# Kernel optimization log

Measured on AMD Instinct MI355X. Metric: run time of the kernel, lower is better.

## Reference

```python
import jax, jax.numpy as jnp
import numpy as np
import math

H = 16          # head_count
D = 1024        # model_dim
DT = 100        # topic_dim
DH = D // H     # dim_per_head


def _lin(x, W, b):
    return x @ W.T + b


def _shape(x, B):
    # [B, L, D] -> [B, H, L, DH]
    return x.reshape(B, -1, H, DH).transpose(0, 2, 1, 3)


def setup_inputs() -> dict:
    key = jax.random.key(0)
    ks = jax.random.split(key, 20)
    B, L = 4, 1024
    s = 0.02
    inp = {
        'key': jax.random.normal(ks[0], (B, L, D), jnp.float32),
        'value': jax.random.normal(ks[1], (B, L, D), jnp.float32),
        'query': jax.random.normal(ks[2], (B, L, D), jnp.float32),
        'mask': jax.random.randint(ks[3], (B, L, L), 0, 2).astype(bool),
        'topic_vec': jax.random.normal(ks[4], (B, L, DT), jnp.float32),
        'Wq': jax.random.normal(ks[5], (D, D), jnp.float32) * s,
        'bq': jnp.zeros((D,), jnp.float32),
        'Wk': jax.random.normal(ks[6], (D, D), jnp.float32) * s,
        'bk': jnp.zeros((D,), jnp.float32),
        'Wv': jax.random.normal(ks[7], (D, D), jnp.float32) * s,
        'bv': jnp.zeros((D,), jnp.float32),
        'Wtk': jax.random.normal(ks[8], (D, D), jnp.float32) * s,
        'btk': jnp.zeros((D,), jnp.float32),
        'Wtv': jax.random.normal(ks[9], (D, DT), jnp.float32) * s,
        'btv': jnp.zeros((D,), jnp.float32),
        'Wtw': jax.random.normal(ks[10], (H, 3 * D), jnp.float32) * s,
        'btw': jnp.zeros((H,), jnp.float32),
        'Wo': jax.random.normal(ks[11], (D, D), jnp.float32) * s,
        'bo': jnp.zeros((D,), jnp.float32),
    }
    return inp


def reference(key, value, query, mask, topic_vec,
              Wq, bq, Wk, bk, Wv, bv, Wtk, btk, Wtv, btv, Wtw, btw, Wo, bo):
    B = key.shape[0]
    # content and topic projections
    q_lin = _lin(query, Wq, bq)          # [B, L, D]
    k_lin = _lin(key, Wk, bk)
    v_lin = _lin(value, Wv, bv)
    tk_lin = _lin(key, Wtk, btk)         # topic keys from key states
    tv_lin = _lin(topic_vec, Wtv, btv)   # topic queries from topic distribution

    q = _shape(q_lin, B) / math.sqrt(DH)   # [B, H, Lq, DH]
    k = _shape(k_lin, B)
    v = _shape(v_lin, B)
    tk = _shape(tk_lin, B)
    tq = _shape(tv_lin, B) / math.sqrt(DH)

    scores = jnp.einsum('bhqd,bhkd->bhqk', q, k)          # content scores
    topic_scores = jnp.einsum('bhqd,bhkd->bhqk', tq, tk)  # topic scores

    # per-query, per-head mixing gate from concatenated projections (3*D -> H)
    gate = jax.nn.sigmoid(_lin(jnp.concatenate([q_lin, tk_lin, tv_lin], axis=-1), Wtw, btw))  # [B, L, H]
    p = gate.transpose(0, 2, 1)[..., None]                # [B, H, Lq, 1]
    scores = (1.0 - p) * scores + p * topic_scores

    # masked_fill(mask, -1e18), mask broadcast over heads
    scores = jnp.where(mask[:, None, :, :], -1e18, scores)
    attn = jax.nn.softmax(scores, axis=-1)
    # dropout is identity at eval time
    ctx = jnp.einsum('bhqk,bhkd->bhqd', attn, v)
    ctx = ctx.transpose(0, 2, 1, 3).reshape(B, -1, D)     # unshape
    return ctx @ Wo.T + bo
```

## Files before the change

### kernel.cpp

```cpp
#include <hip/hip_runtime.h>
#include <hip/hip_bf16.h>

#define BB 4
#define LL 1024
#define DD 1024
#define HH 16
#define DHH 64
#define DTT 100
#define ML (BB*LL)
#define LOG2E 1.4426950408889634f

typedef float f32x4 __attribute__((ext_vector_type(4)));
typedef short s16x8 __attribute__((ext_vector_type(8)));

__device__ __forceinline__ unsigned short f2bf(float x) {
    unsigned u = __builtin_bit_cast(unsigned, x);
    return (unsigned short)((u + 0x7FFFu + ((u >> 16) & 1u)) >> 16);
}
__device__ __forceinline__ unsigned short f2bf_fast(float x) {
    return (unsigned short)((__builtin_bit_cast(unsigned, x) + 0x8000u) >> 16);
}
__device__ __forceinline__ unsigned cvt_pk_bf16(float lo, float hi) {
    unsigned r;
    asm("v_cvt_pk_bf16_f32 %0, %1, %2" : "=v"(r) : "v"(lo), "v"(hi));
    return r;
}
__device__ __forceinline__ float bflo(unsigned u) { return __builtin_bit_cast(float, u << 16); }
__device__ __forceinline__ float bfhi(unsigned u) { return __builtin_bit_cast(float, u & 0xFFFF0000u); }
__device__ __forceinline__ int4 pack_bf16x8(float4 x0, float4 x1) {
    int4 o;
    o.x = cvt_pk_bf16(x0.x, x0.y); o.y = cvt_pk_bf16(x0.z, x0.w);
    o.z = cvt_pk_bf16(x1.x, x1.y); o.w = cvt_pk_bf16(x1.z, x1.w);
    return o;
}
__device__ __forceinline__ void gl_lds16(const unsigned short* g, char* l) {
    __builtin_amdgcn_global_load_lds(
        (const __attribute__((address_space(1))) unsigned*)g,
        (__attribute__((address_space(3))) unsigned*)l, 16, 0, 0);
}

__global__ __launch_bounds__(256)
void conv_fused(const float* __restrict__ qf, const float* __restrict__ kf,
                const float* __restrict__ vf,
                unsigned short* __restrict__ qb, unsigned short* __restrict__ kb,
                unsigned short* __restrict__ vb,
                const float* __restrict__ w0, const float* __restrict__ w1,
                const float* __restrict__ w2, const float* __restrict__ w3,
                const float* __restrict__ w4, unsigned short* __restrict__ wd,
                const float* __restrict__ wtw, unsigned short* __restrict__ wtwd,
                const float* __restrict__ wtv, unsigned short* __restrict__ wtvd,
                const float* __restrict__ topic, unsigned short* __restrict__ topicd,
                const int* __restrict__ mask, unsigned long long* __restrict__ MB) {
    const int bx0 = blockIdx.x, tid = threadIdx.x;
    if (bx0 < 6144) {
        const int which = bx0 >> 11;
        const float* src = which == 0 ? qf : (which == 1 ? kf : vf);
        unsigned short* dst = which == 0 ? qb : (which == 1 ? kb : vb);
        const int idx = (bx0 & 2047) * 256 + tid;
        float4 f0 = *(const float4*)(src + (size_t)idx * 8);
        float4 f1 = *(const float4*)(src + (size_t)idx * 8 + 4);
        *(int4*)(dst + (size_t)idx * 8) = pack_bf16x8(f0, f1);
        return;
    }
    const int bx = bx0 - 6144;
    if (bx < 2560) {
        const int which = bx >> 9;
        const float* src;
        switch (which) {
            case 0:  src = w0; break;
            case 1:  src = w1; break;
            case 2:  src = w2; break;
            case 3:  src = w3; break;
            default: src = w4; break;
        }
        unsigned short* dst = wd + (size_t)which * DD * DD;
        const int idx = (bx & 511) * 256 + tid;
        float4 f0 = *(const float4*)(src + (size_t)idx * 8);
        float4 f1 = *(const float4*)(src + (size_t)idx * 8 + 4);
        *(int4*)(dst + (size_t)idx * 8) = pack_bf16x8(f0, f1);
    } else if (bx < 2584) {
        const int idx = (bx - 2560) * 256 + tid;
        float4 f0 = *(const float4*)(wtw + (size_t)idx * 8);
        float4 f1 = *(const float4*)(wtw + (size_t)idx * 8 + 4);
        *(int4*)(wtwd + (size_t)idx * 8) = pack_bf16x8(f0, f1);
    } else if (bx < 2648) {
        const int idx = (bx - 2584) * 256 + tid;
        const int r = idx >> 4, c0 = (idx & 15) * 8;
        unsigned short o[8];
        #pragma unroll
        for (int j = 0; j < 8; j++) {
            int c = c0 + j;
            o[j] = (c < DTT) ? f2bf(wtv[(size_t)r * DTT + c]) : (unsigned short)0;
        }
        int4 v;
        v.x = o[0] | ((unsigned)o[1] << 16);
        v.y = o[2] | ((unsigned)o[3] << 16);
        v.z = o[4] | ((unsigned)o[5] << 16);
        v.w = o[6] | ((unsigned)o[7] << 16);
        *(int4*)(wtvd + (size_t)r * 128 + c0) = v;
    } else if (bx < 2904) {
        const int idx = (bx - 2648) * 256 + tid;
        const int r = idx >> 4, c0 = (idx & 15) * 8;
        unsigned short o[8];
        #pragma unroll
        for (int j = 0; j < 8; j++) {
            int c = c0 + j;
            o[j] = (c < DTT) ? f2bf(topic[(size_t)r * DTT + c]) : (unsigned short)0;
        }
        int4 v;
        v.x = o[0] | ((unsigned)o[1] << 16);
        v.y = o[2] | ((unsigned)o[3] << 16);
        v.z = o[4] | ((unsigned)o[5] << 16);
        v.w = o[6] | ((unsigned)o[7] << 16);
        *(int4*)(topicd + (size_t)r * 128 + c0) = v;
    } else {
        const int ww = (bx - 2904) * 4 + (tid >> 6);
        const int lane = tid & 63;
        int v = mask[(size_t)ww * 64 + lane];
        unsigned long long bits = __ballot(v != 0);
        if (lane == 0) MB[ww] = bits;
    }
}

struct GArg { const void* A; const unsigned short* W; const float* bias; void* C; int mode; };

#define STAGE256(kt_, Ad_, Bd_) { \
    const unsigned short* agp_ = Ag + (size_t)(kt_) * 64; \
    const unsigned short* bgp_ = Bg + (size_t)(kt_) * 64; \
    _Pragma("unroll") \
    for (int i_ = 0; i_ < 4; i_++) { \
        gl_lds16(agp_ + (size_t)(i_ * 64) * K, (Ad_) + i_ * 8192 + ldst); \
        gl_lds16(bgp_ + (size_t)(i_ * 64) * K, (Bd_) + i_ * 8192 + ldst); \
    } }

__global__ __launch_bounds__(512, 2)
void gemm256(GArg a0, GArg a1, GArg a2, GArg a3, int N, int K) {
    __shared__ char lds[131072];

    const int nb = gridDim.x * gridDim.y * gridDim.z;
    const int flat = blockIdx.x + gridDim.x * (blockIdx.y + gridDim.y * blockIdx.z);
    const int wid = (flat & 7) * (nb >> 3) + (flat >> 3);
    const int bx = wid % gridDim.x;
    const int rem = wid / gridDim.x;
    const int by = rem % gridDim.y;
    const int bz = rem / gridDim.y;

    GArg a;
    switch (bz) {
        case 0:  a = a0; break;
        case 1:  a = a1; break;
        case 2:  a = a2; break;
        default: a = a3; break;
    }

    const int tid = threadIdx.x, w = tid >> 6, l = tid & 63;
    const int g = l >> 4, c = l & 15;
    const int wm = w >> 2, wn = w & 3;
    const int bm = by * 256, bn = bx * 256;
    const int NK = K >> 6;

    const int srow = tid >> 3;
    const int scol = (tid & 7) ^ (srow & 7);
    const unsigned short* const Ag = (const unsigned short*)a.A + (size_t)(bm + srow) * K + scol * 8;
    const unsigned short* const Bg = a.W + (size_t)(bn + srow) * K + scol * 8;
    const int ldst = tid * 16;

    f32x4 acc[8][4];
    #pragma unroll
    for (int m = 0; m < 8; m++)
        #pragma unroll
        for (int n = 0; n < 4; n++)
            #pragma unroll
            for (int j = 0; j < 4; j++) acc[m][n][j] = 0.f;

    STAGE256(0, lds, lds + 32768)
    if (NK > 1) STAGE256(1, lds + 65536, lds + 98304)

    for (int kt = 0; kt < NK; kt++) {
        char* Ab = lds + (kt & 1) * 65536;
        char* Bb = Ab + 32768;
        if (kt + 1 < NK) { asm volatile("s_waitcnt vmcnt(8)" ::: "memory"); }
        else             { asm volatile("s_waitcnt vmcnt(0)" ::: "memory"); }
        __builtin_amdgcn_sched_barrier(0);
        __builtin_amdgcn_s_barrier();
        __builtin_amdgcn_sched_barrier(0);

        s16x8 bfr[4][2];
        #pragma unroll
        for (int n = 0; n < 4; n++) {
            const int rb = wn * 64 + n * 16 + c;
            #pragma unroll
            for (int ks = 0; ks < 2; ks++)
                bfr[n][ks] = *(const s16x8*)(Bb + rb * 128 + (((ks * 4 + g) ^ (rb & 7)) << 4));
        }
        #pragma unroll
        for (int p = 0; p < 4; p++) {
            s16x8 af[2][2];
            #pragma unroll
            for (int mm = 0; mm < 2; mm++) {
                const int ra = wm * 128 + (p * 2 + mm) * 16 + c;
                #pragma unroll
                for (int ks = 0; ks < 2; ks++)
                    af[mm][ks] = *(const s16x8*)(Ab + ra * 128 + (((ks * 4 + g) ^ (ra & 7)) << 4));
            }
            #pragma unroll
            for (int mm = 0; mm < 2; mm++)
                #pragma unroll
                for (int n = 0; n < 4; n++) {
                    acc[p * 2 + mm][n] = __builtin_amdgcn_mfma_f32_16x16x32_bf16(af[mm][0], bfr[n][0], acc[p * 2 + mm][n], 0, 0, 0);
                    acc[p * 2 + mm][n] = __builtin_amdgcn_mfma_f32_16x16x32_bf16(af[mm][1], bfr[n][1], acc[p * 2 + mm][n], 0, 0, 0);
                }
        }
        asm volatile("s_waitcnt lgkmcnt(0)" ::: "memory");
        __builtin_amdgcn_sched_barrier(0);
        __builtin_amdgcn_s_barrier();
        __builtin_amdgcn_sched_barrier(0);
        if (kt + 2 < NK) STAGE256(kt + 2, Ab, Bb)
    }

    const int mode = a.mode;
    if (mode == 1) {
        unsigned short* C = (unsigned short*)a.C;
        #pragma unroll
        for (int n = 0; n < 4; n++) {
            const int col = bn + wn * 64 + n * 16 + c;
            const float bv = a.bias[col];
            #pragma unroll
            for (int m = 0; m < 8; m++) {
                const int row = bm + wm * 128 + m * 16 + g * 4;
                #pragma unroll
                for (int j = 0; j < 4; j++)
                    C[(size_t)(row + j) * N + col] = f2bf(acc[m][n][j] + bv);
            }
        }
    } else if (mode == 2 || mode == 3) {
        unsigned short* C = (unsigned short*)a.C;
        const int off = (mode == 2) ? 0 : 64;
        #pragma unroll
        for (int n = 0; n < 4; n++) {
            const int col = bn + wn * 64 + n * 16 + c;
            const float bv = a.bias[col];
            const int h = col >> 6, d = col & 63;
            #pragma unroll
            for (int m = 0; m < 8; m++) {
                const int row = bm + wm * 128 + m * 16 + g * 4;
                #pragma unroll
                for (int j = 0; j < 4; j++) {
                    const int rr = row + j;
                    C[((size_t)((rr >> 10) * HH + h) * LL + (rr & 1023)) * 128 + off + d] =
                        f2bf(acc[m][n][j] + bv);
                }
            }
        }
    } else {
        unsigned short* C = (unsigned short*)a.C;
        #pragma unroll
        for (int n = 0; n < 4; n++) {
            const int col = bn + wn * 64 + n * 16 + c;
            const float bv = a.bias[col];
            const int h = col >> 6, d = col & 63;
            #pragma unroll
            for (int m = 0; m < 8; m++) {
                const int row = bm + wm * 128 + m * 16 + g * 4;
                unsigned lo = cvt_pk_bf16(acc[m][n][0] + bv, acc[m][n][1] + bv);
                unsigned hi = cvt_pk_bf16(acc[m][n][2] + bv, acc[m][n][3] + bv);
                unsigned long long pk = (unsigned long long)lo | ((unsigned long long)hi << 32);
                *(unsigned long long*)(C + ((size_t)((row >> 10) * HH + h) * 64 + d) * LL + (row & 1023)) = pk;
            }
        }
    }
}

#define LOADW(s0_,s1_,s2_,s3_,kk) \
    s0_ = *(const int4*)(Wb + (kk)); \
    s1_ = *(const int4*)(Wb + (kk) + wstep); \
    s2_ = *(const int4*)(Wb + (kk) + 2 * wstep); \
    s3_ = *(const int4*)(Wb + (kk) + 3 * wstep);
#define STOREW(s0_,s1_,s2_,s3_) \
    *(int4*)(bsl)         = s0_; \
    *(int4*)(bsl + 4096)  = s1_; \
    *(int4*)(bsl + 8192)  = s2_; \
    *(int4*)(bsl + 12288) = s3_;
#define LOADA16(s0_,s1_,s2_,s3_,kk) \
    s0_ = *(const int4*)(Ab16 + (kk)); \
    s1_ = *(const int4*)(Ab16 + (kk) + wstep); \
    s2_ = *(const int4*)(Ab16 + (kk) + 2 * wstep); \
    s3_ = *(const int4*)(Ab16 + (kk) + 3 * wstep);
#define STOREA16(s0_,s1_,s2_,s3_) \
    *(int4*)(asl)         = s0_; \
    *(int4*)(asl + 4096)  = s1_; \
    *(int4*)(asl + 8192)  = s2_; \
    *(int4*)(asl + 12288) = s3_;
#define GEMM_COMPUTE(ABASE, BBASE) \
    _Pragma("unroll") \
    for (int ks = 0; ks < 2; ks++) { \
        s16x8 af[4], bf[4]; \
        _Pragma("unroll") \
        for (int m = 0; m < 4; m++) { \
            const int ra = wr * 64 + m * 16 + c; \
            af[m] = *(const s16x8*)((ABASE) + ra * 128 + (((ks * 4 + g) ^ (ra & 7)) << 4)); \
            const int rb = wc * 64 + m * 16 + c; \
            bf[m] = *(const s16x8*)((BBASE) + rb * 128 + (((ks * 4 + g) ^ (rb & 7)) << 4)); \
        } \
        _Pragma("unroll") \
        for (int m = 0; m < 4; m++) \
            _Pragma("unroll") \
            for (int n = 0; n < 4; n++) \
                acc[m][n] = __builtin_amdgcn_mfma_f32_16x16x32_bf16(af[m], bf[n], acc[m][n], 0, 0, 0); \
    }

__global__ __launch_bounds__(256, 3)
void gemm_mfma(GArg a0, GArg a1, GArg a2, GArg a3, int N, int K) {
    __shared__ char lds[32768];
    char* As = lds;
    char* Bs = lds + 16384;

    const int nb = gridDim.x * gridDim.y * gridDim.z;
    const int flat = blockIdx.x + gridDim.x * (blockIdx.y + gridDim.y * blockIdx.z);
    const int wid = (flat & 7) * (nb >> 3) + (flat >> 3);
    const int bx = wid % gridDim.x;
    const int rem = wid / gridDim.x;
    const int by = rem % gridDim.y;
    const int bz = rem / gridDim.y;

    GArg a;
    switch (bz) {
        case 0:  a = a0; break;
        case 1:  a = a1; break;
        case 2:  a = a2; break;
        default: a = a3; break;
    }

    const int tid = threadIdx.x, w = tid >> 6, l = tid & 63;
    const int g = l >> 4, c = l & 15;
    const int wr = w >> 1, wc = w & 1;
    const int bm = by * 128, bn = bx * 128;

    const int r0 = tid >> 3, sl = tid & 7;
    char* const asl = As + r0 * 128 + ((sl ^ (r0 & 7)) << 4);
    char* const bsl = Bs + r0 * 128 + ((sl ^ (r0 & 7)) << 4);
    const size_t wstep = (size_t)32 * K;
    const unsigned short* const Wb   = a.W + (size_t)(bn + r0) * K + sl * 8;
    const unsigned short* const Ab16 = (const unsigned short*)a.A + (size_t)(bm + r0) * K + sl * 8;

    f32x4 acc[4][4];
    #pragma unroll
    for (int m = 0; m < 4; m++)
        #pragma unroll
        for (int n = 0; n < 4; n++)
            #pragma unroll
            for (int j = 0; j < 4; j++) acc[m][n][j] = 0.f;

    int4 pw0, pw1, pw2, pw3;
    int4 pa0, pa1, pa2, pa3;
    LOADW(pw0, pw1, pw2, pw3, 0)
    LOADA16(pa0, pa1, pa2, pa3, 0)

    for (int k0 = 0; k0 < K; k0 += 64) {
        __syncthreads();
        STOREA16(pa0, pa1, pa2, pa3)
        STOREW(pw0, pw1, pw2, pw3)
        {
            const int kn = (k0 + 64 < K) ? (k0 + 64) : 0;
            LOADW(pw0, pw1, pw2, pw3, kn)
            LOADA16(pa0, pa1, pa2, pa3, kn)
        }
        __syncthreads();
        GEMM_COMPUTE(As, Bs)
    }

    const int mode = a.mode;
    if (mode == 0) {
        float* C = (float*)a.C;
        #pragma unroll
        for (int n = 0; n < 4; n++) {
            const int col = bn + wc * 64 + n * 16 + c;
            const float bv = a.bias[col];
            #pragma unroll
            for (int m = 0; m < 4; m++) {
                const int row = bm + wr * 64 + m * 16 + g * 4;
                #pragma unroll
                for (int j = 0; j < 4; j++)
                    C[(size_t)(row + j) * N + col] = acc[m][n][j] + bv;
            }
        }
    } else {
        unsigned short* C = (unsigned short*)a.C;
        #pragma unroll
        for (int n = 0; n < 4; n++) {
            const int col = bn + wc * 64 + n * 16 + c;
            const float bv = a.bias[col];
            #pragma unroll
            for (int m = 0; m < 4; m++) {
                const int row = bm + wr * 64 + m * 16 + g * 4;
                #pragma unroll
                for (int j = 0; j < 4; j++)
                    C[(size_t)(row + j) * N + col] = f2bf(acc[m][n][j] + bv);
            }
        }
    }
}

__global__ __launch_bounds__(256)
void gate_kernel(const unsigned short* __restrict__ QLb,
                 const unsigned short* __restrict__ KCb,
                 const unsigned short* __restrict__ TVLb,
                 const unsigned short* __restrict__ Wtwb,
                 const float* __restrict__ btw, float* __restrict__ GATE) {
    const int t = threadIdx.x;
    const int q = t >> 6, sub = t & 63, row = sub >> 4, h = sub & 15;
    const int row_g = blockIdx.x * 4 + row;
    const int b = row_g >> 10, l = row_g & 1023;

    float acc = 0.f;
    const unsigned short* wp = Wtwb + h * 3 * DD + q * 768;
    #pragma unroll 4
    for (int cc = 0; cc < 96; cc++) {
        const int i = q * 768 + cc * 8;
        const unsigned short* xp;
        if (i < 1024) {
            xp = QLb + (size_t)row_g * DD + i;
        } else if (i < 2048) {
            const int j = i - 1024;
            xp = KCb + ((size_t)(b * HH + (j >> 6)) * LL + l) * 128 + 64 + (j & 63);
        } else {
            xp = TVLb + (size_t)row_g * DD + (i - 2048);
        }
        int4 xv = *(const int4*)xp;
        int4 wv = *(const int4*)(wp + cc * 8);
        const unsigned xs[4] = {(unsigned)xv.x, (unsigned)xv.y, (unsigned)xv.z, (unsigned)xv.w};
        const unsigned ws[4] = {(unsigned)wv.x, (unsigned)wv.y, (unsigned)wv.z, (unsigned)wv.w};
        #pragma unroll
        for (int jj = 0; jj < 4; jj++) {
            acc = fmaf(bflo(xs[jj]), bflo(ws[jj]), acc);
            acc = fmaf(bfhi(xs[jj]), bfhi(ws[jj]), acc);
        }
    }
    __shared__ float part[4][4][16];
    part[q][row][h] = acc;
    __syncthreads();
    if (t < 64) {
        float s = part[0][row][h] + part[1][row][h] + part[2][row][h] + part[3][row][h] + btw[h];
        GATE[(size_t)row_g * HH + h] = 1.f / (1.f + __expf(-s));
    }
}

__global__ __launch_bounds__(256, 3)
void attn_mfma(const unsigned short* __restrict__ QLb,
               const unsigned short* __restrict__ TVLb,
               const float* __restrict__ GATE,
               const unsigned short* __restrict__ KC,
               const unsigned short* __restrict__ VT,
               const unsigned long long* __restrict__ MB,
               unsigned short* __restrict__ CTb) {
    __shared__ char lds[32768];
    char* kc_l = lds;
    char* vt_l = lds + 16384;
    char* p_l  = lds + 24576;

    const int tid = threadIdx.x, w = tid >> 6, l = tid & 63;
    const int g = l >> 4, c = l & 15;
    const int flat = blockIdx.y * gridDim.x + blockIdx.x;
    const int wid = (flat & 7) * 128 + (flat >> 3);
    const int qb = wid & 15, bh = wid >> 4;
    const int b = bh >> 4, h = bh & 15;
    const int q0 = qb * 64;

    const size_t kcg = (size_t)bh * LL * 128;
    const size_t vtg = (size_t)bh * 64 * LL;

    const int kr = tid >> 4, ks = tid & 15;
    const size_t kgo = (size_t)kr * 128 + ks * 8;
    char* const klb = kc_l + kr * 256 + ((ks ^ (kr & 7)) << 4);
    const int vr = tid >> 3, vs = tid & 7;
    const size_t vgo = (size_t)vr * LL + vs * 8;
    char* const vlb = vt_l + vr * 128 + ((vs ^ (vr & 7)) << 4);

    int4 pk0, pk1, pk2, pk3, pv0, pv1;
    {
        const unsigned short* kp = KC + kcg + kgo;
        pk0 = *(const int4*)kp;
        pk1 = *(const int4*)(kp + 16 * 128);
        pk2 = *(const int4*)(kp + 32 * 128);
        pk3 = *(const int4*)(kp + 48 * 128);
        const unsigned short* vp = VT + vtg + vgo;
        pv0 = *(const int4*)vp;
        pv1 = *(const int4*)(vp + 32 * LL);
    }

    {
        const size_t rowbase = (size_t)b * LL + q0 + kr;
        const unsigned short* qsrc =
            (ks < 8 ? QLb : TVLb) + rowbase * DD + h * DHH + (ks & 7) * 8;
        const float* gp = GATE + rowbase * HH + h;
        #pragma unroll
        for (int i = 0; i < 4; i++) {
            const float p = gp[(size_t)i * 16 * HH];
            const float sc = (ks < 8 ? 1.f - p : p) * (0.125f * LOG2E);
            int4 v = *(const int4*)(qsrc + (size_t)i * 16 * DD);
            int4 o;
            o.x = cvt_pk_bf16(bflo((unsigned)v.x) * sc, bfhi((unsigned)v.x) * sc);
            o.y = cvt_pk_bf16(bflo((unsigned)v.y) * sc, bfhi((unsigned)v.y) * sc);
            o.z = cvt_pk_bf16(bflo((unsigned)v.z) * sc, bfhi((unsigned)v.z) * sc);
            o.w = cvt_pk_bf16(bflo((unsigned)v.w) * sc, bfhi((unsigned)v.w) * sc);
            *(int4*)(klb + i * 4096) = o;
        }
    }
    __syncthreads();
    s16x8 qf[4];
    const int ql = w * 16 + c;
    #pragma unroll
    for (int kss = 0; kss < 4; kss++) {
        int t = kss * 4 + g;
        qf[kss] = *(s16x8*)(kc_l + ql * 256 + ((t ^ (ql & 7)) << 4));
    }

    f32x4 ctx[4], la;
    #pragma unroll
    for (int ct = 0; ct < 4; ct++)
        #pragma unroll
        for (int j = 0; j < 4; j++) ctx[ct][j] = 0.f;
    #pragma unroll
    for (int j = 0; j < 4; j++) la[j] = 0.f;
    float m_s = -1e18f;

    s16x8 ones;
    #pragma unroll
    for (int j = 0; j < 8; j++) ones[j] = (short)0x3F80;

    const unsigned long long* mbq = MB + ((size_t)b * LL + q0 + w * 16 + c) * 16;

    for (int kt = 0; kt < 16; kt++) {
        __syncthreads();
        *(int4*)(klb)          = pk0;
        *(int4*)(klb + 4096)   = pk1;
        *(int4*)(klb + 8192)   = pk2;
        *(int4*)(klb + 12288)  = pk3;
        *(int4*)(vlb)          = pv0;
        *(int4*)(vlb + 4096)   = pv1;
        {
            const unsigned short* kp = KC + kcg + (size_t)(kt + 1) * (64 * 128) + kgo;
            pk0 = *(const int4*)kp;
            pk1 = *(const int4*)(kp + 16 * 128);
            pk2 = *(const int4*)(kp + 32 * 128);
            pk3 = *(const int4*)(kp + 48 * 128);
            const unsigned short* vp = VT + vtg + (size_t)(kt + 1) * 64 + vgo;
            pv0 = *(const int4*)vp;
            pv1 = *(const int4*)(vp + 32 * LL);
        }
        __syncthreads();

        f32x4 sf[4];
        #pragma unroll
        for (int ct = 0; ct < 4; ct++) {
            f32x4 acc;
            #pragma unroll
            for (int j = 0; j < 4; j++) acc[j] = 0.f;
            const int rk = ct * 16 + c;
            #pragma unroll
            for (int kss = 0; kss < 4; kss++) {
                int t = kss * 4 + g;
                s16x8 kf = *(s16x8*)(kc_l + rk * 256 + ((t ^ (rk & 7)) << 4));
                acc = __builtin_amdgcn_mfma_f32_16x16x32_bf16(kf, qf[kss], acc, 0, 0, 0);
            }
            sf[ct] = acc;
        }

        {
            const unsigned long long mw = mbq[kt];
            const unsigned ms0 = (unsigned)(mw >> (g * 4));
            const unsigned ms1 = (unsigned)(mw >> (g * 4 + 32));
            #pragma unroll
            for (int ct = 0; ct < 4; ct++) {
                const unsigned mm = (ct & 2) ? ms1 : ms0;
                const int sh = (ct & 1) ? 16 : 0;
                #pragma unroll
                for (int j = 0; j < 4; j++)
                    if ((mm >> (sh + j)) & 1u) sf[ct][j] = -1e18f;
            }
            float t0 = fmaxf(fmaxf(sf[0][0], sf[0][1]), fmaxf(sf[0][2], sf[0][3]));
            float t1 = fmaxf(fmaxf(sf[1][0], sf[1][1]), fmaxf(sf[1][2], sf[1][3]));
            float t2 = fmaxf(fmaxf(sf[2][0], sf[2][1]), fmaxf(sf[2][2], sf[2][3]));
            float t3 = fmaxf(fmaxf(sf[3][0], sf[3][1]), fmaxf(sf[3][2], sf[3][3]));
            float mx = fmaxf(fmaxf(t0, t1), fmaxf(t2, t3));
            mx = fmaxf(mx, __shfl_xor(mx, 16));
            mx = fmaxf(mx, __shfl_xor(mx, 32));
            const float mn = fmaxf(m_s, mx);
            const float cf = exp2f(m_s - mn);
            m_s = mn;

            const float cr0 = __shfl(cf, g * 4 + 0, 16);
            const float cr1 = __shfl(cf, g * 4 + 1, 16);
            const float cr2 = __shfl(cf, g * 4 + 2, 16);
            const float cr3 = __shfl(cf, g * 4 + 3, 16);
            #pragma unroll
            for (int ct = 0; ct < 4; ct++) {
                ctx[ct][0] *= cr0; ctx[ct][1] *= cr1;
                ctx[ct][2] *= cr2; ctx[ct][3] *= cr3;
            }
            la[0] *= cr0; la[1] *= cr1; la[2] *= cr2; la[3] *= cr3;

            char* pw = p_l + w * 2048 + c * 128;
            #pragma unroll
            for (int ct = 0; ct < 4; ct++) {
                const unsigned lo = cvt_pk_bf16(exp2f(sf[ct][0] - mn), exp2f(sf[ct][1] - mn));
                const unsigned hi = cvt_pk_bf16(exp2f(sf[ct][2] - mn), exp2f(sf[ct][3] - mn));
                const unsigned long long pkv =
                    (unsigned long long)lo | ((unsigned long long)hi << 32);
                *(unsigned long long*)(pw + (((ct * 2 + (g >> 1)) ^ (c & 7)) << 4) + ((g & 1) << 3)) = pkv;
            }
        }

        char* pb = p_l + w * 2048;
        s16x8 pa0 = *(s16x8*)(pb + c * 128 + (((0 + g) ^ (c & 7)) << 4));
        s16x8 pa1 = *(s16x8*)(pb + c * 128 + (((4 + g) ^ (c & 7)) << 4));
        #pragma unroll
        for (int ct = 0; ct < 4; ct++) {
            const int dv = ct * 16 + c;
            s16x8 v0 = *(s16x8*)(vt_l + dv * 128 + (((0 + g) ^ (dv & 7)) << 4));
            s16x8 v1 = *(s16x8*)(vt_l + dv * 128 + (((4 + g) ^ (dv & 7)) << 4));
            ctx[ct] = __builtin_amdgcn_mfma_f32_16x16x32_bf16(pa0, v0, ctx[ct], 0, 0, 0);
            ctx[ct] = __builtin_amdgcn_mfma_f32_16x16x32_bf16(pa1, v1, ctx[ct], 0, 0, 0);
        }
        la = __builtin_amdgcn_mfma_f32_16x16x32_bf16(pa0, ones, la, 0, 0, 0);
        la = __builtin_amdgcn_mfma_f32_16x16x32_bf16(pa1, ones, la, 0, 0, 0);
    }

    #pragma unroll
    for (int r = 0; r < 4; r++) {
        const float inv = 1.f / la[r];
        const int q = q0 + w * 16 + g * 4 + r;
        unsigned short* dst = CTb + ((size_t)b * LL + q) * DD + h * DHH + c;
        dst[0]  = f2bf(ctx[0][r] * inv);
        dst[16] = f2bf(ctx[1][r] * inv);
        dst[32] = f2bf(ctx[2][r] * inv);
        dst[48] = f2bf(ctx[3][r] * inv);
    }
}

extern "C" void kernel_launch(void* const* d_in, const int* in_sizes, int n_in,
                              void* d_out, int out_size, void* d_ws, size_t ws_size,
                              hipStream_t stream) {
    const float* key   = (const float*)d_in[0];
    const float* value = (const float*)d_in[1];
    const float* query = (const float*)d_in[2];
    const int*   mask  = (const int*)d_in[3];
    const float* topic = (const float*)d_in[4];
    const float* Wq  = (const float*)d_in[5];  const float* bq  = (const float*)d_in[6];
    const float* Wk  = (const float*)d_in[7];  const float* bk  = (const float*)d_in[8];
    const float* Wv  = (const float*)d_in[9];  const float* bv  = (const float*)d_in[10];
    const float* Wtk = (const float*)d_in[11]; const float* btk = (const float*)d_in[12];
    const float* Wtv = (const float*)d_in[13]; const float* btv = (const float*)d_in[14];
    const float* Wtw = (const float*)d_in[15]; const float* btw = (const float*)d_in[16];
    const float* Wo  = (const float*)d_in[17]; const float* bo  = (const float*)d_in[18];
    float* out = (float*)d_out;

    const size_t NTOK = (size_t)ML * DD;
    unsigned short* Wqb   = (unsigned short*)d_ws;
    unsigned short* Wkb   = Wqb  + (size_t)DD * DD;
    unsigned short* Wvb   = Wkb  + (size_t)DD * DD;
    unsigned short* Wtkb  = Wvb  + (size_t)DD * DD;
    unsigned short* Wob   = Wtkb + (size_t)DD * DD;
    unsigned short* Wtvb  = Wob  + (size_t)DD * DD;
    unsigned short* Wtwb  = Wtvb + (size_t)DD * 128;
    unsigned short* topicb= Wtwb + (size_t)HH * 3 * DD;
    unsigned short* QLb   = topicb + (size_t)ML * 128;
    unsigned short* TVLb  = QLb  + NTOK;
    unsigned short* CTb   = TVLb + NTOK;
    unsigned short* KCb   = CTb  + NTOK;
    unsigned short* VTb   = KCb  + (size_t)BB * HH * LL * 128;
    float* GATE           = (float*)(VTb + (size_t)BB * HH * 64 * LL);
    unsigned long long* MBp = (unsigned long long*)(GATE + (size_t)ML * HH);
    unsigned short* QBb   = (unsigned short*)(MBp + (size_t)BB * LL * LL / 64);
    unsigned short* KBb   = QBb + NTOK;
    unsigned short* VBb   = KBb + NTOK;

    conv_fused<<<25432, 256, 0, stream>>>(query, key, value, QBb, KBb, VBb,
                                          Wq, Wk, Wv, Wtk, Wo, Wqb,
                                          Wtw, Wtwb, Wtv, Wtvb, topic, topicb,
                                          mask, MBp);

    gemm256<<<dim3(DD / 256, ML / 256, 4), 512, 0, stream>>>(
        GArg{QBb, Wqb,  bq,  QLb, 1},
        GArg{KBb, Wkb,  bk,  KCb, 2},
        GArg{VBb, Wvb,  bv,  VTb, 4},
        GArg{KBb, Wtkb, btk, KCb, 3},
        DD, DD);
    gemm_mfma<<<dim3(DD / 128, ML / 128, 1), 256, 0, stream>>>(
        GArg{topicb, Wtvb, btv, TVLb, 1},
        GArg{topicb, Wtvb, btv, TVLb, 1},
        GArg{topicb, Wtvb, btv, TVLb, 1},
        GArg{topicb, Wtvb, btv, TVLb, 1},
        DD, 128);

    gate_kernel<<<ML / 4, 256, 0, stream>>>(QLb, KCb, TVLb, Wtwb, btw, GATE);

    attn_mfma<<<dim3(LL / 64, BB * HH), 256, 0, stream>>>(QLb, TVLb, GATE, KCb, VTb, MBp, CTb);

    gemm_mfma<<<dim3(DD / 128, ML / 128, 1), 256, 0, stream>>>(
        GArg{CTb, Wob, bo, out, 0},
        GArg{CTb, Wob, bo, out, 0},
        GArg{CTb, Wob, bo, out, 0},
        GArg{CTb, Wob, bo, out, 0},
        DD, DD);
}
```

Before: 198.9 us.

## Overlap next-stage global loads with second half-K MFMAs and prefetch mask words

In the main bf16 GEMM loop, the A fragments are split by k-half. The second-half A fragments are read before the barrier so the next STAGE256 global-to-LDS loads can be issued before the second batch of MFMAs, overlapping memory traffic with compute. Plain __syncthreads in the other GEMM and the attention kernel are replaced by an explicit lgkmcnt wait plus s_barrier wrapped in sched barriers. The attention loop also prefetches the next tile's mask word one iteration ahead. This holds more A registers live and constrains the compiler's scheduling around barriers.

```diff
diff --git a/kernel.cpp b/kernel.cpp
--- a/kernel.cpp
+++ b/kernel.cpp
@@ -37,6 +37,13 @@
     __builtin_amdgcn_global_load_lds(
         (const __attribute__((address_space(1))) unsigned*)g,
         (__attribute__((address_space(3))) unsigned*)l, 16, 0, 0);
+}
+__device__ __forceinline__ void barrier_lgkm() {
+    __builtin_amdgcn_sched_barrier(0);
+    asm volatile("s_waitcnt lgkmcnt(0)" ::: "memory");
+    __builtin_amdgcn_sched_barrier(0);
+    __builtin_amdgcn_s_barrier();
+    __builtin_amdgcn_sched_barrier(0);
 }
 
 __global__ __launch_bounds__(256)
@@ -193,29 +200,30 @@
             for (int ks = 0; ks < 2; ks++)
                 bfr[n][ks] = *(const s16x8*)(Bb + rb * 128 + (((ks * 4 + g) ^ (rb & 7)) << 4));
         }
-        #pragma unroll
-        for (int p = 0; p < 4; p++) {
-            s16x8 af[2][2];
-            #pragma unroll
-            for (int mm = 0; mm < 2; mm++) {
-                const int ra = wm * 128 + (p * 2 + mm) * 16 + c;
-                #pragma unroll
-                for (int ks = 0; ks < 2; ks++)
-                    af[mm][ks] = *(const s16x8*)(Ab + ra * 128 + (((ks * 4 + g) ^ (ra & 7)) << 4));
-            }
-            #pragma unroll
-            for (int mm = 0; mm < 2; mm++)
-                #pragma unroll
-                for (int n = 0; n < 4; n++) {
-                    acc[p * 2 + mm][n] = __builtin_amdgcn_mfma_f32_16x16x32_bf16(af[mm][0], bfr[n][0], acc[p * 2 + mm][n], 0, 0, 0);
-                    acc[p * 2 + mm][n] = __builtin_amdgcn_mfma_f32_16x16x32_bf16(af[mm][1], bfr[n][1], acc[p * 2 + mm][n], 0, 0, 0);
-                }
-        }
-        asm volatile("s_waitcnt lgkmcnt(0)" ::: "memory");
-        __builtin_amdgcn_sched_barrier(0);
-        __builtin_amdgcn_s_barrier();
-        __builtin_amdgcn_sched_barrier(0);
+        s16x8 a0[8];
+        #pragma unroll
+        for (int m = 0; m < 8; m++) {
+            const int ra = wm * 128 + m * 16 + c;
+            a0[m] = *(const s16x8*)(Ab + ra * 128 + ((g ^ (ra & 7)) << 4));
+        }
+        #pragma unroll
+        for (int m = 0; m < 8; m++)
+            #pragma unroll
+            for (int n = 0; n < 4; n++)
+                acc[m][n] = __builtin_amdgcn_mfma_f32_16x16x32_bf16(a0[m], bfr[n][0], acc[m][n], 0, 0, 0);
+        s16x8 a1[8];
+        #pragma unroll
+        for (int m = 0; m < 8; m++) {
+            const int ra = wm * 128 + m * 16 + c;
+            a1[m] = *(const s16x8*)(Ab + ra * 128 + (((4 + g) ^ (ra & 7)) << 4));
+        }
+        barrier_lgkm();
         if (kt + 2 < NK) STAGE256(kt + 2, Ab, Bb)
+        #pragma unroll
+        for (int m = 0; m < 8; m++)
+            #pragma unroll
+            for (int n = 0; n < 4; n++)
+                acc[m][n] = __builtin_amdgcn_mfma_f32_16x16x32_bf16(a1[m], bfr[n][1], acc[m][n], 0, 0, 0);
     }
 
     const int mode = a.mode;
@@ -357,7 +365,7 @@
     LOADA16(pa0, pa1, pa2, pa3, 0)
 
     for (int k0 = 0; k0 < K; k0 += 64) {
-        __syncthreads();
+        barrier_lgkm();
         STOREA16(pa0, pa1, pa2, pa3)
         STOREW(pw0, pw1, pw2, pw3)
         {
@@ -365,7 +373,7 @@
             LOADW(pw0, pw1, pw2, pw3, kn)
             LOADA16(pa0, pa1, pa2, pa3, kn)
         }
-        __syncthreads();
+        barrier_lgkm();
         GEMM_COMPUTE(As, Bs)
     }
 
@@ -506,7 +514,7 @@
             *(int4*)(klb + i * 4096) = o;
         }
     }
-    __syncthreads();
+    barrier_lgkm();
     s16x8 qf[4];
     const int ql = w * 16 + c;
     #pragma unroll
@@ -529,15 +537,17 @@
     for (int j = 0; j < 8; j++) ones[j] = (short)0x3F80;
 
     const unsigned long long* mbq = MB + ((size_t)b * LL + q0 + w * 16 + c) * 16;
+    unsigned long long mw_cur = mbq[0];
 
     for (int kt = 0; kt < 16; kt++) {
-        __syncthreads();
+        barrier_lgkm();
         *(int4*)(klb)          = pk0;
         *(int4*)(klb + 4096)   = pk1;
         *(int4*)(klb + 8192)   = pk2;
         *(int4*)(klb + 12288)  = pk3;
         *(int4*)(vlb)          = pv0;
         *(int4*)(vlb + 4096)   = pv1;
+        unsigned long long mw_nxt;
         {
             const unsigned short* kp = KC + kcg + (size_t)(kt + 1) * (64 * 128) + kgo;
             pk0 = *(const int4*)kp;
@@ -547,8 +557,9 @@
             const unsigned short* vp = VT + vtg + (size_t)(kt + 1) * 64 + vgo;
             pv0 = *(const int4*)vp;
             pv1 = *(const int4*)(vp + 32 * LL);
-        }
-        __syncthreads();
+            mw_nxt = mbq[kt + 1 < 16 ? kt + 1 : 15];
+        }
+        barrier_lgkm();
 
         f32x4 sf[4];
         #pragma unroll
@@ -567,7 +578,8 @@
         }
 
         {
-            const unsigned long long mw = mbq[kt];
+            const unsigned long long mw = mw_cur;
+            mw_cur = mw_nxt;
             const unsigned ms0 = (unsigned)(mw >> (g * 4));
             const unsigned ms1 = (unsigned)(mw >> (g * 4 + 32));
             #pragma unroll
```

Result: no change. 199.9 us (+0.5%).
